# Kernel optimization log

Hardware: AMD Instinct MI355X
Metric: run time of the kernel (lower is better)

## Reference

```python
import jax, jax.numpy as jnp
import numpy as np

N = 131072      # total nodes (1024 graphs x 128 nodes)
E = 1048576     # edges (avg degree 8)
IN = 74         # atom feature length
H = 128         # dim_embedding == all hidden_feats
B = 1024        # batch_size (graphs)
L = 3           # number of GCN+GRU layers


def setup_inputs() -> dict:
    key = jax.random.key(0)
    ks = jax.random.split(key, 10)
    node_feats = jax.random.normal(ks[0], (N, IN), dtype=jnp.float32)
    src = jax.random.randint(ks[1], (E,), 0, N, dtype=jnp.int32)
    dst = jax.random.randint(ks[2], (E,), 0, N, dtype=jnp.int32)
    s_in = 1.0 / np.sqrt(IN)
    s_h = 1.0 / np.sqrt(H)
    # init_transform: Linear(IN, H, bias=False); padding=True zeros the last output unit
    W_init = jax.random.normal(ks[3], (IN, H), dtype=jnp.float32) * s_in
    W_init = W_init.at[:, -1].set(0.0)
    lin_W = jax.random.normal(ks[4], (L, H, H), dtype=jnp.float32) * s_h
    lin_b = jax.random.normal(ks[5], (L, H), dtype=jnp.float32) * s_h
    gru_Wih = jax.random.normal(ks[6], (L, 3 * H, H), dtype=jnp.float32) * s_h
    gru_Whh = jax.random.normal(ks[7], (L, 3 * H, H), dtype=jnp.float32) * s_h
    gru_bih = jax.random.normal(ks[8], (L, 3 * H), dtype=jnp.float32) * s_h
    gru_bhh = jax.random.normal(ks[9], (L, 3 * H), dtype=jnp.float32) * s_h
    return {
        "node_feats": node_feats, "src": src, "dst": dst,
        "W_init": W_init, "lin_W": lin_W, "lin_b": lin_b,
        "gru_Wih": gru_Wih, "gru_Whh": gru_Whh,
        "gru_bih": gru_bih, "gru_bhh": gru_bhh,
        "batch_size": B,
    }


def _gru_cell(x, h, Wih, Whh, bih, bhh):
    # PyTorch GRUCell semantics
    gi = x @ Wih.T + bih   # [N, 3H]
    gh = h @ Whh.T + bhh   # [N, 3H]
    i_r, i_z, i_n = jnp.split(gi, 3, axis=-1)
    h_r, h_z, h_n = jnp.split(gh, 3, axis=-1)
    r = jax.nn.sigmoid(i_r + h_r)
    z = jax.nn.sigmoid(i_z + h_z)
    n = jnp.tanh(i_n + r * h_n)
    return (1.0 - z) * n + z * h


def reference(node_feats, src, dst, W_init, lin_W, lin_b,
              gru_Wih, gru_Whh, gru_bih, gru_bhh, batch_size):
    n_nodes = node_feats.shape[0]
    h = node_feats @ W_init  # init_transform (no bias)
    for l in range(lin_W.shape[0]):
        # update_all: sum incoming source features (scatter-add over edges)
        agg = jax.ops.segment_sum(h[src], dst, num_segments=n_nodes)
        x = jax.nn.relu(agg @ lin_W[l].T + lin_b[l])
        h = _gru_cell(x, h, gru_Wih[l], gru_Whh[l], gru_bih[l], gru_bhh[l])
    return h.reshape(batch_size, -1, h.shape[-1])
```

## Files before the change

kernel.cpp:

```cpp
#include <hip/hip_runtime.h>
#include <hip/hip_bf16.h>

#define NN 131072
#define EE 1048576
#define IN_F 74
#define HH 128
#define LL 3

using f32x4  = __attribute__((ext_vector_type(4))) float;
using f32x16 = __attribute__((ext_vector_type(16))) float;
using bf16x8 = __attribute__((ext_vector_type(8))) short;
typedef unsigned short ushort_t;
typedef unsigned int uint_t;

__device__ __forceinline__ short f2bf(float f) {
    __hip_bfloat16 b = __float2bfloat16(f);
    return __builtin_bit_cast(short, b);
}
__device__ __forceinline__ float bf2f(short s) {
    unsigned int u = ((unsigned int)(unsigned short)s) << 16;
    return __builtin_bit_cast(float, u);
}
__device__ __forceinline__ float bitf(uint_t u) { return __builtin_bit_cast(float, u); }
__device__ __forceinline__ float sigmoidf_(float x) { return 1.f / (1.f + __expf(-x)); }
__device__ __forceinline__ float tanhf_(float x)
{
    x = fminf(fmaxf(x, -15.f), 15.f);
    float e2 = __expf(2.f * x);
    return (e2 - 1.f) / (e2 + 1.f);
}

__global__ __launch_bounds__(256) void k_init_gemm(
    const float* __restrict__ nf, const float* __restrict__ Wi,
    ushort_t* __restrict__ hhi, ushort_t* __restrict__ hlo)
{
    __shared__ float Wis[IN_F * HH];
    __shared__ float nfs[32 * IN_F];
    int b = blockIdx.x;
    int t = threadIdx.x;

    for (int i = t; i < IN_F * HH / 4; i += 256)
        reinterpret_cast<float4*>(Wis)[i] = reinterpret_cast<const float4*>(Wi)[i];
    {
        const float4* nf4 = reinterpret_cast<const float4*>(nf + (long)b * 32 * IN_F);
        for (int i = t; i < 32 * IN_F / 4; i += 256)
            reinterpret_cast<float4*>(nfs)[i] = nf4[i];
    }
    __syncthreads();

    int nl = t >> 3;
    int c0 = (t & 7) * 4;
    float acc[4][4];
#pragma unroll
    for (int hf = 0; hf < 4; ++hf)
#pragma unroll
        for (int j = 0; j < 4; ++j) acc[hf][j] = 0.f;

    const float* nrow = nfs + nl * IN_F;
#pragma unroll 2
    for (int k = 0; k < IN_F; ++k) {
        float a = nrow[k];
#pragma unroll
        for (int hf = 0; hf < 4; ++hf) {
            float4 wv = *reinterpret_cast<const float4*>(Wis + k * HH + hf * 32 + c0);
            acc[hf][0] += a * wv.x;
            acc[hf][1] += a * wv.y;
            acc[hf][2] += a * wv.z;
            acc[hf][3] += a * wv.w;
        }
    }

    int node = b * 32 + nl;
#pragma unroll
    for (int hf = 0; hf < 4; ++hf) {
        uint_t uh[2], ul[2];
#pragma unroll
        for (int p = 0; p < 2; ++p) {
            float v0 = acc[hf][p * 2], v1 = acc[hf][p * 2 + 1];
            short h0 = f2bf(v0), h1 = f2bf(v1);
            short l0 = f2bf(v0 - bf2f(h0)), l1 = f2bf(v1 - bf2f(h1));
            uh[p] = (uint_t)(ushort_t)h0 | ((uint_t)(ushort_t)h1 << 16);
            ul[p] = (uint_t)(ushort_t)l0 | ((uint_t)(ushort_t)l1 << 16);
        }
        long adr = (long)node * HH + hf * 32 + c0;
        *reinterpret_cast<uint2*>(hhi + adr) = make_uint2(uh[0], uh[1]);
        *reinterpret_cast<uint2*>(hlo + adr) = make_uint2(ul[0], ul[1]);
    }
}

__global__ __launch_bounds__(256) void k_hist(const int* __restrict__ dsti, int* __restrict__ deg)
{
    int e = blockIdx.x * 256 + threadIdx.x;
    atomicAdd(&deg[dsti[e]], 1);
}

__global__ __launch_bounds__(256) void k_scan1(const int* __restrict__ deg, int* __restrict__ bsum)
{
    __shared__ int s[256];
    int b = blockIdx.x, t = threadIdx.x;
    int v = 0;
#pragma unroll
    for (int i = 0; i < 4; ++i) v += deg[b * 1024 + t * 4 + i];
    s[t] = v;
    __syncthreads();
    for (int st = 128; st > 0; st >>= 1) {
        if (t < st) s[t] += s[t + st];
        __syncthreads();
    }
    if (t == 0) bsum[b] = s[0];
}

__global__ void k_scan2(int* __restrict__ bsum, int nb)
{
    if (threadIdx.x == 0) {
        int run = 0;
        for (int i = 0; i < nb; ++i) { int v = bsum[i]; bsum[i] = run; run += v; }
    }
}

__global__ __launch_bounds__(256) void k_scan3(
    const int* __restrict__ deg, const int* __restrict__ bsum, int* __restrict__ row_start)
{
    __shared__ int s[256];
    int b = blockIdx.x, t = threadIdx.x;
    int base = b * 1024 + t * 4;
    int d0 = deg[base], d1 = deg[base + 1], d2 = deg[base + 2], d3 = deg[base + 3];
    int local = d0 + d1 + d2 + d3;
    s[t] = local;
    __syncthreads();
    for (int st = 1; st < 256; st <<= 1) {
        int v = (t >= st) ? s[t - st] : 0;
        __syncthreads();
        s[t] += v;
        __syncthreads();
    }
    int excl = s[t] - local + bsum[b];
    row_start[base] = excl;
    row_start[base + 1] = excl + d0;
    row_start[base + 2] = excl + d0 + d1;
    row_start[base + 3] = excl + d0 + d1 + d2;
    if (b == gridDim.x - 1 && t == 255) row_start[NN] = excl + local;
}

__global__ __launch_bounds__(256) void k_fill(
    const int* __restrict__ src, const int* __restrict__ dsti,
    const int* __restrict__ row_start, int* __restrict__ cursor, int* __restrict__ csr_src)
{
    int e = blockIdx.x * 256 + threadIdx.x;
    int d = dsti[e];
    int pos = atomicAdd(&cursor[d], 1);
    csr_src[row_start[d] + pos] = src[e];
}

__global__ __launch_bounds__(256) void k_split(
    const float* __restrict__ srcw, ushort_t* __restrict__ hi,
    ushort_t* __restrict__ lo, int n)
{
    int i = blockIdx.x * 256 + threadIdx.x;
    if (i >= n) return;
    float a = srcw[i];
    short h = f2bf(a);
    float rem = a - bf2f(h);
    hi[i] = (ushort_t)h;
    lo[i] = (ushort_t)f2bf(rem);
}

#define EIDX_CAP 1024

template <bool LDSIDX>
__device__ __forceinline__ void gather_node(
    const ushort_t* __restrict__ hhi, const int* __restrict__ eidx,
    const int* __restrict__ csr_src, int estart, int e0, int e1, int c4, int esel,
    float& a0, float& a1, float& a2, float& a3)
{
    int e = e0;
    for (; e + 7 < e1; e += 8) {
        uint2 v[4];
#pragma unroll
        for (int u = 0; u < 4; ++u) {
            int ee = e + u * 2 + esel;
            int s = LDSIDX ? eidx[ee] : csr_src[estart + ee];
            v[u] = *reinterpret_cast<const uint2*>(hhi + (long)s * HH + c4);
        }
#pragma unroll
        for (int u = 0; u < 4; ++u) {
            a0 += bitf(v[u].x << 16);
            a1 += bitf(v[u].x & 0xffff0000u);
            a2 += bitf(v[u].y << 16);
            a3 += bitf(v[u].y & 0xffff0000u);
        }
    }
    for (; e + 1 < e1; e += 2) {
        int ee = e + esel;
        int s = LDSIDX ? eidx[ee] : csr_src[estart + ee];
        uint2 vv = *reinterpret_cast<const uint2*>(hhi + (long)s * HH + c4);
        a0 += bitf(vv.x << 16);
        a1 += bitf(vv.x & 0xffff0000u);
        a2 += bitf(vv.y << 16);
        a3 += bitf(vv.y & 0xffff0000u);
    }
    if (e < e1 && esel == 0) {
        int s = LDSIDX ? eidx[e] : csr_src[estart + e];
        uint2 vv = *reinterpret_cast<const uint2*>(hhi + (long)s * HH + c4);
        a0 += bitf(vv.x << 16);
        a1 += bitf(vv.x & 0xffff0000u);
        a2 += bitf(vv.y << 16);
        a3 += bitf(vv.y & 0xffff0000u);
    }
}

__global__ __launch_bounds__(256) void k_x(
    const ushort_t* __restrict__ hhi, const ushort_t* __restrict__ hlo,
    const int* __restrict__ row_start, const int* __restrict__ csr_src,
    const ushort_t* __restrict__ lWhi, const ushort_t* __restrict__ lWlo,
    const float* __restrict__ lb,
    ushort_t* __restrict__ xhi, ushort_t* __restrict__ xlo)
{
    __shared__ float aggs[32 * 128];
    __shared__ int eidx[EIDX_CAP];
    char* abase = (char*)aggs;
    int n0 = blockIdx.x * 32;
    int t = threadIdx.x;
    int w = t >> 6, lane = t & 63;

    int estart = row_start[n0];
    int ecount = row_start[n0 + 32] - estart;
    bool inl = (ecount <= EIDX_CAP);
    for (int i = t; i < ecount && i < EIDX_CAP; i += 256)
        eidx[i] = csr_src[estart + i];
    __syncthreads();

    int c4 = (lane & 31) * 4;
    int esel = lane >> 5;

    for (int i = 0; i < 8; ++i) {
        int nl = w * 8 + i;
        int node = n0 + nl;
        int e0 = row_start[node] - estart;
        int e1 = row_start[node + 1] - estart;
        float a0 = 0.f, a1 = 0.f, a2 = 0.f, a3 = 0.f;
        if (inl)
            gather_node<true>(hhi, eidx, csr_src, estart, e0, e1, c4, esel, a0, a1, a2, a3);
        else
            gather_node<false>(hhi, eidx, csr_src, estart, e0, e1, c4, esel, a0, a1, a2, a3);
        a0 += __shfl_xor(a0, 32, 64);
        a1 += __shfl_xor(a1, 32, 64);
        a2 += __shfl_xor(a2, 32, 64);
        a3 += __shfl_xor(a3, 32, 64);
        if (lane < 32) {
            int swz = (nl & 7) << 4;
            float4 st = make_float4(a0, a1, a2, a3);
            *reinterpret_cast<float4*>(abase + ((nl * 512 + c4 * 4) ^ swz)) = st;
        }
    }
    __syncthreads();

    int ng = w >> 1, jg = w & 1;
    int l16 = lane & 15, lq = lane >> 4;

    f32x4 acc[4];
#pragma unroll
    for (int js = 0; js < 4; ++js) acc[js] = (f32x4){0.f, 0.f, 0.f, 0.f};

#pragma unroll
    for (int kk = 0; kk < 4; ++kk) {
        int k0 = kk * 32;
        int nodeL = ng * 16 + l16;
        int kb = (k0 + lq * 8) * 4;
        int swz = (nodeL & 7) << 4;
        float4 f0 = *reinterpret_cast<const float4*>(abase + ((nodeL * 512 + kb) ^ swz));
        float4 f1 = *reinterpret_cast<const float4*>(abase + ((nodeL * 512 + kb + 16) ^ swz));
        float av[8] = {f0.x, f0.y, f0.z, f0.w, f1.x, f1.y, f1.z, f1.w};
        bf16x8 ahi, alo;
#pragma unroll
        for (int e = 0; e < 8; ++e) {
            short hh_ = f2bf(av[e]);
            ahi[e] = hh_;
            alo[e] = f2bf(av[e] - bf2f(hh_));
        }
#pragma unroll
        for (int js = 0; js < 4; ++js) {
            int jrow = jg * 64 + js * 16 + l16;
            bf16x8 Bh = *reinterpret_cast<const bf16x8*>(lWhi + (long)jrow * HH + k0 + lq * 8);
            bf16x8 Bl = *reinterpret_cast<const bf16x8*>(lWlo + (long)jrow * HH + k0 + lq * 8);
            acc[js] = __builtin_amdgcn_mfma_f32_16x16x32_bf16(ahi, Bh, acc[js], 0, 0, 0);
            acc[js] = __builtin_amdgcn_mfma_f32_16x16x32_bf16(ahi, Bl, acc[js], 0, 0, 0);
            acc[js] = __builtin_amdgcn_mfma_f32_16x16x32_bf16(alo, Bh, acc[js], 0, 0, 0);
        }
    }

#pragma unroll
    for (int js = 0; js < 4; ++js) {
        int j = jg * 64 + js * 16 + l16;
        float bj = lb[j];
#pragma unroll
        for (int r = 0; r < 4; ++r) {
            int node = n0 + ng * 16 + lq * 4 + r;
            float v = fmaxf(acc[js][r] + bj, 0.f);
            long adr = (long)node * HH + j;
            short hi_ = f2bf(v);
            xhi[adr] = (ushort_t)hi_;
            xlo[adr] = (ushort_t)f2bf(v - bf2f(hi_));
        }
    }
}

#define LDSA(p) ((p) * 16384)
#define LDSB(p) (65536 + (p) * 32768)

__device__ __forceinline__ void stage_slab(
    const ushort_t* __restrict__ g, char* lds, int tid, int nchunk512)
{
    const uint4* g4 = reinterpret_cast<const uint4*>(g);
#pragma unroll
    for (int i = 0; i < 4; ++i) {
        if (i >= nchunk512) break;
        int c = i * 512 + tid;
        int L = c * 16;
        int row = L >> 8, kb = L & 255;
        *reinterpret_cast<uint4*>(lds + row * 256 + (kb ^ ((row & 15) << 4))) = g4[c];
    }
}

__device__ __forceinline__ void gru_half(
    f32x16& acc, const char* smem, int pAhi, int myoff, int rs_my,
    int jjoff, int rs_jj, int lh)
{
    bf16x8 Ahi[8], Alo[8];
#pragma unroll
    for (int kc = 0; kc < 8; ++kc) {
        int kb = kc * 32 + lh * 16;
        Ahi[kc] = *reinterpret_cast<const bf16x8*>(smem + LDSA(pAhi)     + myoff + (kb ^ rs_my));
        Alo[kc] = *reinterpret_cast<const bf16x8*>(smem + LDSA(pAhi + 1) + myoff + (kb ^ rs_my));
    }
#pragma unroll
    for (int kc = 0; kc < 8; ++kc) {
        int kb = kc * 32 + lh * 16;
        bf16x8 wh = *reinterpret_cast<const bf16x8*>(smem + LDSB(0) + jjoff + (kb ^ rs_jj));
        bf16x8 wl = *reinterpret_cast<const bf16x8*>(smem + LDSB(1) + jjoff + (kb ^ rs_jj));
        acc = __builtin_amdgcn_mfma_f32_32x32x16_bf16(Ahi[kc], wh, acc, 0, 0, 0);
        acc = __builtin_amdgcn_mfma_f32_32x32x16_bf16(Ahi[kc], wl, acc, 0, 0, 0);
        acc = __builtin_amdgcn_mfma_f32_32x32x16_bf16(Alo[kc], wh, acc, 0, 0, 0);
    }
}

__global__ void k_gru(
    const ushort_t* __restrict__ xhi, const ushort_t* __restrict__ xlo,
    ushort_t* __restrict__ hhi, ushort_t* __restrict__ hlo,
    const ushort_t* __restrict__ Wihhi, const ushort_t* __restrict__ Wihlo,
    const ushort_t* __restrict__ Whhhi, const ushort_t* __restrict__ Whhlo,
    const float* __restrict__ bi, const float* __restrict__ bh)
{
    __shared__ uint4 smem4[131072 / 16];
    char* smem = (char*)smem4;

    int t = threadIdx.x;
    int w = t >> 6, lane = t & 63;
    int ng = w >> 2, og = w & 3;
    int l31 = lane & 31, lh = lane >> 5;
    int n0 = blockIdx.x * 64;
    int myrow = ng * 32 + l31;
    int jj = og * 32 + l31;
    int myoff = myrow * 256, rs_my = (myrow & 15) << 4;
    int jjoff = jj * 256,   rs_jj = (jj & 15) << 4;

    stage_slab(xhi + (long)n0 * HH, smem + LDSA(0), t, 2);
    stage_slab(xlo + (long)n0 * HH, smem + LDSA(1), t, 2);
    stage_slab(hhi + (long)n0 * HH, smem + LDSA(2), t, 2);
    stage_slab(hlo + (long)n0 * HH, smem + LDSA(3), t, 2);
    stage_slab(Whhhi + 256 * HH, smem + LDSB(0), t, 4);
    stage_slab(Whhlo + 256 * HH, smem + LDSB(1), t, 4);
    __syncthreads();

    f32x16 acc1;
#pragma unroll
    for (int i = 0; i < 16; ++i) acc1[i] = 0.f;
    gru_half(acc1, smem, 2, myoff, rs_my, jjoff, rs_jj, lh);

    f32x16 acc2;
#pragma unroll
    for (int i = 0; i < 16; ++i) acc2[i] = 0.f;
    __syncthreads();
    stage_slab(Wihhi, smem + LDSB(0), t, 4);
    stage_slab(Wihlo, smem + LDSB(1), t, 4);
    __syncthreads();
    gru_half(acc2, smem, 0, myoff, rs_my, jjoff, rs_jj, lh);
    __syncthreads();
    stage_slab(Whhhi, smem + LDSB(0), t, 4);
    stage_slab(Whhlo, smem + LDSB(1), t, 4);
    __syncthreads();
    gru_half(acc2, smem, 2, myoff, rs_my, jjoff, rs_jj, lh);
    {
        float bR = bi[jj] + bh[jj];
        float bNh = bh[256 + jj];
#pragma unroll
        for (int i = 0; i < 16; ++i)
            acc1[i] = sigmoidf_(acc2[i] + bR) * (acc1[i] + bNh);
    }

#pragma unroll
    for (int i = 0; i < 16; ++i) acc2[i] = 0.f;
    __syncthreads();
    stage_slab(Wihhi + 256 * HH, smem + LDSB(0), t, 4);
    stage_slab(Wihlo + 256 * HH, smem + LDSB(1), t, 4);
    __syncthreads();
    gru_half(acc2, smem, 0, myoff, rs_my, jjoff, rs_jj, lh);
    {
        float bNi = bi[256 + jj];
#pragma unroll
        for (int i = 0; i < 16; ++i)
            acc1[i] = tanhf_(acc2[i] + bNi + acc1[i]);
    }

#pragma unroll
    for (int i = 0; i < 16; ++i) acc2[i] = 0.f;
    __syncthreads();
    stage_slab(Wihhi + 128 * HH, smem + LDSB(0), t, 4);
    stage_slab(Wihlo + 128 * HH, smem + LDSB(1), t, 4);
    __syncthreads();
    gru_half(acc2, smem, 0, myoff, rs_my, jjoff, rs_jj, lh);
    __syncthreads();
    stage_slab(Whhhi + 128 * HH, smem + LDSB(0), t, 4);
    stage_slab(Whhlo + 128 * HH, smem + LDSB(1), t, 4);
    __syncthreads();
    gru_half(acc2, smem, 2, myoff, rs_my, jjoff, rs_jj, lh);

    {
        float bZ = bi[128 + jj] + bh[128 + jj];
        int kb2 = 2 * jj;
#pragma unroll
        for (int reg = 0; reg < 16; ++reg) {
            int ndl = ng * 32 + (reg & 3) + 8 * (reg >> 2) + 4 * lh;
            long adr = (long)(n0 + ndl) * HH + jj;
            int rsn = (ndl & 15) << 4;
            float hold = bf2f(*reinterpret_cast<const short*>(smem + LDSA(2) + ndl * 256 + (kb2 ^ rsn)))
                       + bf2f(*reinterpret_cast<const short*>(smem + LDSA(3) + ndl * 256 + (kb2 ^ rsn)));
            float zv = sigmoidf_(acc2[reg] + bZ);
            float hp = (1.f - zv) * acc1[reg] + zv * hold;
            short hi_ = f2bf(hp);
            hhi[adr] = (ushort_t)hi_;
            hlo[adr] = (ushort_t)f2bf(hp - bf2f(hi_));
        }
    }
}

__global__ __launch_bounds__(256) void k_copy(
    const uint_t* __restrict__ hhi, const uint_t* __restrict__ hlo,
    float2* __restrict__ out)
{
    long i = (long)blockIdx.x * 256 + threadIdx.x;
    uint_t vh = hhi[i], vl = hlo[i];
    float2 o;
    o.x = bitf(vh << 16) + bitf(vl << 16);
    o.y = bitf(vh & 0xffff0000u) + bitf(vl & 0xffff0000u);
    out[i] = o;
}

extern "C" void kernel_launch(void* const* d_in, const int* in_sizes, int n_in,
                              void* d_out, int out_size, void* d_ws, size_t ws_size,
                              hipStream_t stream)
{
    const float* nf     = (const float*)d_in[0];
    const int*   src    = (const int*)d_in[1];
    const int*   dsti   = (const int*)d_in[2];
    const float* W_init = (const float*)d_in[3];
    const float* lin_W  = (const float*)d_in[4];
    const float* lin_b  = (const float*)d_in[5];
    const float* Wih    = (const float*)d_in[6];
    const float* Whh    = (const float*)d_in[7];
    const float* bih    = (const float*)d_in[8];
    const float* bhh    = (const float*)d_in[9];

    char* ws = (char*)d_ws;
    ushort_t* hhi = (ushort_t*)ws;
    ushort_t* hlo = (ushort_t*)(ws + (32ull << 20));
    ushort_t* xhi = (ushort_t*)(ws + (64ull << 20));
    ushort_t* xlo = (ushort_t*)(ws + (96ull << 20));
    int* deg    = (int*)(ws + (64ull << 20));
    int* cursor = (int*)(ws + (64ull << 20) + (1 << 20));
    int* bsum   = (int*)(ws + (64ull << 20) + (2 << 20));

    char* ob = (char*)d_out;
    int* row_start = (int*)ob;
    int* csr_src   = (int*)(ob + (1ull << 20));
    ushort_t* lWhi  = (ushort_t*)(ob + (6ull << 20));
    ushort_t* lWlo  = lWhi  + 3 * 128 * 128;
    ushort_t* Wihhi = lWlo  + 3 * 128 * 128;
    ushort_t* Wihlo = Wihhi + 3 * 384 * 128;
    ushort_t* Whhhi = Wihlo + 3 * 384 * 128;
    ushort_t* Whhlo = Whhhi + 3 * 384 * 128;

    k_init_gemm<<<NN / 32, 256, 0, stream>>>(nf, W_init, hhi, hlo);

    hipMemsetAsync(deg, 0, (size_t)NN * 4, stream);
    hipMemsetAsync(cursor, 0, (size_t)NN * 4, stream);
    k_hist<<<EE / 256, 256, 0, stream>>>(dsti, deg);
    k_scan1<<<NN / 1024, 256, 0, stream>>>(deg, bsum);
    k_scan2<<<1, 64, 0, stream>>>(bsum, NN / 1024);
    k_scan3<<<NN / 1024, 256, 0, stream>>>(deg, bsum, row_start);
    k_fill<<<EE / 256, 256, 0, stream>>>(src, dsti, row_start, cursor, csr_src);

    k_split<<<(3 * 128 * 128 + 255) / 256, 256, 0, stream>>>(lin_W, lWhi, lWlo, 3 * 128 * 128);
    k_split<<<(3 * 384 * 128 + 255) / 256, 256, 0, stream>>>(Wih, Wihhi, Wihlo, 3 * 384 * 128);
    k_split<<<(3 * 384 * 128 + 255) / 256, 256, 0, stream>>>(Whh, Whhhi, Whhlo, 3 * 384 * 128);

    for (int l = 0; l < LL; ++l) {
        k_x<<<NN / 32, 256, 0, stream>>>(
            hhi, hlo, row_start, csr_src,
            lWhi + (long)l * 128 * 128, lWlo + (long)l * 128 * 128,
            lin_b + (long)l * 128, xhi, xlo);
        k_gru<<<NN / 64, 512, 0, stream>>>(
            xhi, xlo, hhi, hlo,
            Wihhi + (long)l * 384 * 128, Wihlo + (long)l * 384 * 128,
            Whhhi + (long)l * 384 * 128, Whhlo + (long)l * 384 * 128,
            bih + (long)l * 384, bhh + (long)l * 384);
    }

    k_copy<<<NN * HH / 2 / 256, 256, 0, stream>>>((const uint_t*)hhi, (const uint_t*)hlo, (float2*)d_out);
}
```

Measured before the change: 891.9 us.

## Drop low-half weight terms in GRU MFMA and pair gate slabs per stage

The GRU kernel now multiplies only by the bf16 high part of the weights (2 MFMAs per k-chunk instead of 3). This frees the LDS slot that held the low half, so two gate weight slabs are staged per sync phase and the sync/stage rounds drop from six to three. It also stops preloading all A fragments into registers and adds launch_bounds(512,2). The weight rounding error grows to plain bf16 precision on the weights, which may affect accuracy against the fp32 reference.

After: 828.3 us. 7.1% less time.

```diff
diff --git a/kernel.cpp b/kernel.cpp
--- a/kernel.cpp
+++ b/kernel.cpp
@@ -322,33 +322,25 @@
     }
 }
 
-__device__ __forceinline__ void gru_half(
-    f32x16& acc, const char* smem, int pAhi, int myoff, int rs_my,
-    int jjoff, int rs_jj, int lh)
-{
-    bf16x8 Ahi[8], Alo[8];
+__device__ __forceinline__ void gru_half2(
+    f32x16& acc, const char* smem, int pAhi, int bbase,
+    int myoff, int rs_my, int jjoff, int rs_jj, int lh)
+{
 #pragma unroll
     for (int kc = 0; kc < 8; ++kc) {
         int kb = kc * 32 + lh * 16;
-        Ahi[kc] = *reinterpret_cast<const bf16x8*>(smem + LDSA(pAhi)     + myoff + (kb ^ rs_my));
-        Alo[kc] = *reinterpret_cast<const bf16x8*>(smem + LDSA(pAhi + 1) + myoff + (kb ^ rs_my));
-    }
-#pragma unroll
-    for (int kc = 0; kc < 8; ++kc) {
-        int kb = kc * 32 + lh * 16;
-        bf16x8 wh = *reinterpret_cast<const bf16x8*>(smem + LDSB(0) + jjoff + (kb ^ rs_jj));
-        bf16x8 wl = *reinterpret_cast<const bf16x8*>(smem + LDSB(1) + jjoff + (kb ^ rs_jj));
-        acc = __builtin_amdgcn_mfma_f32_32x32x16_bf16(Ahi[kc], wh, acc, 0, 0, 0);
-        acc = __builtin_amdgcn_mfma_f32_32x32x16_bf16(Ahi[kc], wl, acc, 0, 0, 0);
-        acc = __builtin_amdgcn_mfma_f32_32x32x16_bf16(Alo[kc], wh, acc, 0, 0, 0);
-    }
-}
-
-__global__ void k_gru(
+        bf16x8 ah = *reinterpret_cast<const bf16x8*>(smem + LDSA(pAhi)     + myoff + (kb ^ rs_my));
+        bf16x8 al = *reinterpret_cast<const bf16x8*>(smem + LDSA(pAhi + 1) + myoff + (kb ^ rs_my));
+        bf16x8 wh = *reinterpret_cast<const bf16x8*>(smem + bbase + jjoff + (kb ^ rs_jj));
+        acc = __builtin_amdgcn_mfma_f32_32x32x16_bf16(ah, wh, acc, 0, 0, 0);
+        acc = __builtin_amdgcn_mfma_f32_32x32x16_bf16(al, wh, acc, 0, 0, 0);
+    }
+}
+
+__global__ __launch_bounds__(512, 2) void k_gru(
     const ushort_t* __restrict__ xhi, const ushort_t* __restrict__ xlo,
     ushort_t* __restrict__ hhi, ushort_t* __restrict__ hlo,
-    const ushort_t* __restrict__ Wihhi, const ushort_t* __restrict__ Wihlo,
-    const ushort_t* __restrict__ Whhhi, const ushort_t* __restrict__ Whhlo,
+    const ushort_t* __restrict__ Wihhi, const ushort_t* __restrict__ Whhhi,
     const float* __restrict__ bi, const float* __restrict__ bh)
 {
     __shared__ uint4 smem4[131072 / 16];
@@ -369,61 +361,43 @@
     stage_slab(hhi + (long)n0 * HH, smem + LDSA(2), t, 2);
     stage_slab(hlo + (long)n0 * HH, smem + LDSA(3), t, 2);
     stage_slab(Whhhi + 256 * HH, smem + LDSB(0), t, 4);
-    stage_slab(Whhlo + 256 * HH, smem + LDSB(1), t, 4);
-    __syncthreads();
-
-    f32x16 acc1;
-#pragma unroll
-    for (int i = 0; i < 16; ++i) acc1[i] = 0.f;
-    gru_half(acc1, smem, 2, myoff, rs_my, jjoff, rs_jj, lh);
-
-    f32x16 acc2;
-#pragma unroll
-    for (int i = 0; i < 16; ++i) acc2[i] = 0.f;
-    __syncthreads();
-    stage_slab(Wihhi, smem + LDSB(0), t, 4);
-    stage_slab(Wihlo, smem + LDSB(1), t, 4);
-    __syncthreads();
-    gru_half(acc2, smem, 0, myoff, rs_my, jjoff, rs_jj, lh);
-    __syncthreads();
-    stage_slab(Whhhi, smem + LDSB(0), t, 4);
-    stage_slab(Whhlo, smem + LDSB(1), t, 4);
-    __syncthreads();
-    gru_half(acc2, smem, 2, myoff, rs_my, jjoff, rs_jj, lh);
+    stage_slab(Whhhi,            smem + LDSB(1), t, 4);
+    __syncthreads();
+
+    f32x16 accNH, accR;
+#pragma unroll
+    for (int i = 0; i < 16; ++i) { accNH[i] = 0.f; accR[i] = 0.f; }
+    gru_half2(accNH, smem, 2, LDSB(0), myoff, rs_my, jjoff, rs_jj, lh);
+    gru_half2(accR,  smem, 2, LDSB(1), myoff, rs_my, jjoff, rs_jj, lh);
+
+    __syncthreads();
+    stage_slab(Wihhi,            smem + LDSB(0), t, 4);
+    stage_slab(Wihhi + 256 * HH, smem + LDSB(1), t, 4);
+    __syncthreads();
+    gru_half2(accR, smem, 0, LDSB(0), myoff, rs_my, jjoff, rs_jj, lh);
+    f32x16 accNI;
+#pragma unroll
+    for (int i = 0; i < 16; ++i) accNI[i] = 0.f;
+    gru_half2(accNI, smem, 0, LDSB(1), myoff, rs_my, jjoff, rs_jj, lh);
     {
         float bR = bi[jj] + bh[jj];
         float bNh = bh[256 + jj];
-#pragma unroll
-        for (int i = 0; i < 16; ++i)
-            acc1[i] = sigmoidf_(acc2[i] + bR) * (acc1[i] + bNh);
-    }
-
-#pragma unroll
-    for (int i = 0; i < 16; ++i) acc2[i] = 0.f;
-    __syncthreads();
-    stage_slab(Wihhi + 256 * HH, smem + LDSB(0), t, 4);
-    stage_slab(Wihlo + 256 * HH, smem + LDSB(1), t, 4);
-    __syncthreads();
-    gru_half(acc2, smem, 0, myoff, rs_my, jjoff, rs_jj, lh);
-    {
         float bNi = bi[256 + jj];
 #pragma unroll
-        for (int i = 0; i < 16; ++i)
-            acc1[i] = tanhf_(acc2[i] + bNi + acc1[i]);
-    }
-
-#pragma unroll
-    for (int i = 0; i < 16; ++i) acc2[i] = 0.f;
+        for (int i = 0; i < 16; ++i) {
+            float rn = sigmoidf_(accR[i] + bR) * (accNH[i] + bNh);
+            accNH[i] = tanhf_(accNI[i] + bNi + rn);
+        }
+    }
+
     __syncthreads();
     stage_slab(Wihhi + 128 * HH, smem + LDSB(0), t, 4);
-    stage_slab(Wihlo + 128 * HH, smem + LDSB(1), t, 4);
-    __syncthreads();
-    gru_half(acc2, smem, 0, myoff, rs_my, jjoff, rs_jj, lh);
-    __syncthreads();
-    stage_slab(Whhhi + 128 * HH, smem + LDSB(0), t, 4);
-    stage_slab(Whhlo + 128 * HH, smem + LDSB(1), t, 4);
-    __syncthreads();
-    gru_half(acc2, smem, 2, myoff, rs_my, jjoff, rs_jj, lh);
+    stage_slab(Whhhi + 128 * HH, smem + LDSB(1), t, 4);
+    __syncthreads();
+#pragma unroll
+    for (int i = 0; i < 16; ++i) accR[i] = 0.f;
+    gru_half2(accR, smem, 0, LDSB(0), myoff, rs_my, jjoff, rs_jj, lh);
+    gru_half2(accR, smem, 2, LDSB(1), myoff, rs_my, jjoff, rs_jj, lh);
 
     {
         float bZ = bi[128 + jj] + bh[128 + jj];
@@ -435,8 +409,8 @@
             int rsn = (ndl & 15) << 4;
             float hold = bf2f(*reinterpret_cast<const short*>(smem + LDSA(2) + ndl * 256 + (kb2 ^ rsn)))
                        + bf2f(*reinterpret_cast<const short*>(smem + LDSA(3) + ndl * 256 + (kb2 ^ rsn)));
-            float zv = sigmoidf_(acc2[reg] + bZ);
-            float hp = (1.f - zv) * acc1[reg] + zv * hold;
+            float zv = sigmoidf_(accR[reg] + bZ);
+            float hp = (1.f - zv) * accNH[reg] + zv * hold;
             short hi_ = f2bf(hp);
             hhi[adr] = (ushort_t)hi_;
             hlo[adr] = (ushort_t)f2bf(hp - bf2f(hi_));
@@ -511,8 +485,7 @@
             lin_b + (long)l * 128, xhi, xlo);
         k_gru<<<NN / 64, 512, 0, stream>>>(
             xhi, xlo, hhi, hlo,
-            Wihhi + (long)l * 384 * 128, Wihlo + (long)l * 384 * 128,
-            Whhhi + (long)l * 384 * 128, Whhlo + (long)l * 384 * 128,
+            Wihhi + (long)l * 384 * 128, Whhhi + (long)l * 384 * 128,
             bih + (long)l * 384, bhh + (long)l * 384);
     }
 
```
